# Performance work log

Measured on AMD Instinct MI355X. Metric: run time of the kernel, lower is better.

## Reference

```python
import jax, jax.numpy as jnp
import numpy as np

# Loss hyperparameters (match init_kwargs)
DELTA_VAR = 0.75
DELTA_DIST = 2.0
ALPHA, BETA, GAMMA = 1.0, 1.0, 0.001


def setup_inputs() -> dict:
    key = jax.random.key(0)
    k1, k2 = jax.random.split(key)
    B, C, H, W = 4, 32, 512, 512
    N_INST = 100
    input_ = jax.random.normal(k1, (B, C, H, W), dtype=jnp.float32)
    target = jax.random.randint(k2, (B, 1, H, W), 0, N_INST, dtype=jnp.int64)
    return {"input_": input_, "target": target, "n_instances": N_INST}


def _loss_single(feat, lbl, n_inst):
    # feat: [C, H, W] embeddings for one sample; lbl: [H, W] instance ids in [0, n_inst)
    C = feat.shape[0]
    f = feat.reshape(C, -1).T                     # [P, C] pixel embeddings
    l = lbl.reshape(-1)                           # [P]
    counts = jnp.bincount(l, length=n_inst).astype(f.dtype)     # [n]
    sums = jax.ops.segment_sum(f, l, num_segments=n_inst)       # [n, C]
    means = sums / counts[:, None]                               # cluster means [n, C]

    # variance (attractive) term: hinge on distance of each pixel to its cluster mean
    diff = f - means[l]                           # gather means back to pixels
    var = jnp.linalg.norm(diff, axis=1)           # 'fro' over dim=1 == L2
    var = jnp.clip(var - DELTA_VAR, 0.0) ** 2 / counts[l]
    variance_term = var.sum() / n_inst

    # distance (repulsive) term: hinged pairwise distances between cluster means
    eye = jnp.eye(n_inst, dtype=f.dtype)
    d2 = jnp.sum((means[:, None, :] - means[None, :, :]) ** 2, axis=2)  # [n, n]
    # safe sqrt: diagonal is exactly 0; mask it so grads stay finite, value unchanged
    dmat = jnp.sqrt(jnp.where(d2 > 0, d2, 1.0)) * (1.0 - eye)
    repulsion = 2.0 * DELTA_DIST * (1.0 - eye)
    hinged = jnp.clip(repulsion - dmat, 0.0) ** 2
    distance_term = hinged.sum() / (n_inst * (n_inst - 1))

    # regularization term: pull cluster means toward origin
    reg_term = jnp.linalg.norm(means, axis=1).sum() / n_inst

    return ALPHA * variance_term + BETA * distance_term + GAMMA * reg_term


def reference(input_, target, n_instances):
    # input_: [B, C, H, W], target: [B, 1, H, W]
    lbl = target[:, 0]
    losses = jax.vmap(lambda f, l: _loss_single(f, l, n_instances))(input_, lbl)
    return losses.mean()  # loss.div(n_batches)
```

## Files before the change

kernel.cpp:

```cpp
#include <hip/hip_runtime.h>
#include <math.h>

#define BB 4
#define CC 32
#define HWSZ (512*512)
#define NMAX 128
#define NP 132
#define NP64 133
#define SS (NMAX * CC)

#define PPB 1024
#define CHUNKS (HWSZ / PPB)
#define NBLK (BB * CHUNKS)

#define DSLICE 8

#define DELTA_VAR_C 0.75f
#define DELTA_DIST_C 2.0f
#define GAMMA_C 0.001f
#define FXS 1048576.0f
#define FXI (1.0f / 1048576.0f)
#define BIAS 16777216

#define LD4(p) (*(const float4*)(p))

__device__ __forceinline__ float block_reduce_256(float v, float* red, int tid) {
    #pragma unroll
    for (int o = 32; o > 0; o >>= 1) v += __shfl_down(v, o, 64);
    if ((tid & 63) == 0) red[tid >> 6] = v;
    __syncthreads();
    if (tid == 0) v = red[0] + red[1] + red[2] + red[3];
    return v;
}

__global__ __launch_bounds__(256) void k_seg_sum(
    const float* __restrict__ in, const int* __restrict__ lbl,
    const int* __restrict__ n_ptr, int* __restrict__ sums_i,
    unsigned int* __restrict__ counts_u)
{
    const int N = *n_ptr;
    __shared__ unsigned long long s_sum[(CC / 2) * NP64];
    __shared__ unsigned int s_cnt[NMAX];
    const int tid = threadIdx.x;

    for (int i = tid; i < (CC / 2) * NP64; i += 256) s_sum[i] = 0ull;
    for (int i = tid; i < NMAX; i += 256) s_cnt[i] = 0u;
    __syncthreads();

    const int b = blockIdx.x / CHUNKS;
    const int p0 = (blockIdx.x % CHUNKS) * PPB;

    const int* lb = lbl + (size_t)b * HWSZ + p0 + tid * 4;
    int4 l4 = *(const int4*)(lb);
    int lab[4] = {l4.x, l4.y, l4.z, l4.w};

    #pragma unroll
    for (int i = 0; i < 4; i++) atomicAdd(&s_cnt[lab[i]], 1u);

    const float* p = in + (size_t)b * CC * HWSZ + p0 + (size_t)tid * 4;

    float4 c0a = LD4(p);
    float4 c0b = LD4(p + HWSZ);
    float4 c1a = LD4(p + 2 * (size_t)HWSZ);
    float4 c1b = LD4(p + 3 * (size_t)HWSZ);

    #pragma unroll
    for (int c = 0; c < CC; c += 2) {
        float4 va = c0a, vb = c0b;
        c0a = c1a; c0b = c1b;
        if (c + 4 < CC) {
            const float* q = p + (size_t)(c + 4) * HWSZ;
            c1a = LD4(q);
            c1b = LD4(q + HWSZ);
        }
        float v0[4] = {va.x, va.y, va.z, va.w};
        float v1[4] = {vb.x, vb.y, vb.z, vb.w};
        unsigned long long* row = &s_sum[(c >> 1) * NP64];
        #pragma unroll
        for (int i = 0; i < 4; i++) {
            unsigned int lo = (unsigned int)((int)(v0[i] * FXS) + BIAS);
            unsigned int hi = (unsigned int)((int)(v1[i] * FXS) + BIAS);
            unsigned long long pk = (unsigned long long)lo |
                                    ((unsigned long long)hi << 32);
            atomicAdd(&row[lab[i]], pk);
        }
    }
    __syncthreads();

    for (int i = tid; i < N * CC; i += 256) {
        int n = i / CC, c = i % CC;
        unsigned long long v = s_sum[(c >> 1) * NP64 + n];
        unsigned int half = (c & 1) ? (unsigned int)(v >> 32) : (unsigned int)v;
        long long val = (long long)half - ((long long)s_cnt[n] << 24);
        if (val != 0)
            atomicAdd(&sums_i[(size_t)b * SS + i], (int)val);
    }
    for (int i = tid; i < N; i += 256) {
        unsigned int cv = s_cnt[i];
        if (cv) atomicAdd(&counts_u[b * NMAX + i], cv);
    }
}

__global__ __launch_bounds__(256) void k_var(
    const float* __restrict__ in, const int* __restrict__ lbl,
    const int* __restrict__ n_ptr, const int* __restrict__ sums_i,
    const unsigned int* __restrict__ counts_u, int* __restrict__ out_acc)
{
    const int N = *n_ptr;
    __shared__ float m_t[CC * NP];
    __shared__ float s_invc[NMAX];
    __shared__ float red[4];
    const int tid = threadIdx.x;

    const int b = blockIdx.x / CHUNKS;
    const int chunk = blockIdx.x % CHUNKS;
    const int p0 = chunk * PPB;

    for (int i = tid; i < N; i += 256)
        s_invc[i] = 1.0f / (float)counts_u[b * NMAX + i];
    __syncthreads();
    for (int i = tid; i < N * CC; i += 256) {
        int n = i / CC, c = i % CC;
        m_t[c * NP + n] = (float)sums_i[(size_t)b * SS + i] * FXI * s_invc[n];
    }
    __syncthreads();

    const int* lb = lbl + (size_t)b * HWSZ + p0 + tid * 4;
    int4 l4 = *(const int4*)(lb);
    int lab[4] = {l4.x, l4.y, l4.z, l4.w};
    float acc[4] = {0.f, 0.f, 0.f, 0.f};

    const float* p = in + (size_t)b * CC * HWSZ + p0 + (size_t)tid * 4;
    float4 c0a = LD4(p);
    float4 c0b = LD4(p + HWSZ);
    float4 c1a = LD4(p + 2 * (size_t)HWSZ);
    float4 c1b = LD4(p + 3 * (size_t)HWSZ);

    #pragma unroll
    for (int c = 0; c < CC; c += 2) {
        float4 va = c0a, vb = c0b;
        c0a = c1a; c0b = c1b;
        if (c + 4 < CC) {
            const float* q = p + (size_t)(c + 4) * HWSZ;
            c1a = LD4(q);
            c1b = LD4(q + HWSZ);
        }
        float v0[4] = {va.x, va.y, va.z, va.w};
        #pragma unroll
        for (int i = 0; i < 4; i++) {
            float d = v0[i] - m_t[c * NP + lab[i]];
            acc[i] += d * d;
        }
        float v1[4] = {vb.x, vb.y, vb.z, vb.w};
        #pragma unroll
        for (int i = 0; i < 4; i++) {
            float d = v1[i] - m_t[(c + 1) * NP + lab[i]];
            acc[i] += d * d;
        }
    }

    float vsum = 0.f;
    #pragma unroll
    for (int i = 0; i < 4; i++) {
        float nm = sqrtf(acc[i]);
        float t = fmaxf(nm - DELTA_VAR_C, 0.f);
        vsum += t * t * s_invc[lab[i]];
    }
    float total = vsum * (1.0f / ((float)N * (float)BB));

    if (chunk < DSLICE) {
        float dist_sum = 0.f;
        for (int pr = chunk * 256 + tid; pr < N * N; pr += DSLICE * 256) {
            int i = pr / N, j = pr - i * N;
            if (i == j) continue;
            float d2 = 0.f;
            #pragma unroll
            for (int c = 0; c < CC; c++) {
                float d = m_t[c * NP + i] - m_t[c * NP + j];
                d2 += d * d;
            }
            float dm = (d2 > 0.f) ? sqrtf(d2) : 1.0f;
            float h = fmaxf(2.0f * DELTA_DIST_C - dm, 0.f);
            dist_sum += h * h;
        }
        total += dist_sum * (1.0f / ((float)N * (float)(N - 1) * (float)BB));
        if (chunk == 0) {
            float reg_sum = 0.f;
            for (int n = tid; n < N; n += 256) {
                float s = 0.f;
                #pragma unroll
                for (int c = 0; c < CC; c++) { float v = m_t[c * NP + n]; s += v * v; }
                reg_sum += sqrtf(s);
            }
            total += reg_sum * (GAMMA_C / ((float)N * (float)BB));
        }
    }

    float tot = block_reduce_256(total, red, tid);
    if (tid == 0)
        atomicAdd(out_acc, (int)rintf(tot * FXS));
}

__global__ void k_final(const int* __restrict__ out_acc, float* __restrict__ out) {
    if (threadIdx.x == 0 && blockIdx.x == 0)
        *out = (float)(*out_acc) * FXI;
}

extern "C" void kernel_launch(void* const* d_in, const int* in_sizes, int n_in,
                              void* d_out, int out_size, void* d_ws, size_t ws_size,
                              hipStream_t stream) {
    (void)in_sizes; (void)n_in; (void)out_size; (void)ws_size;
    const float* in  = (const float*)d_in[0];
    const int*   lbl = (const int*)d_in[1];
    const int*   n_ptr = (const int*)d_in[2];
    float* out = (float*)d_out;

    int* sums_i = (int*)d_ws;
    unsigned int* counts_u = (unsigned int*)(sums_i + BB * SS);
    int* out_acc = (int*)(counts_u + BB * NMAX);

    hipMemsetAsync(d_ws, 0, (size_t)(BB * SS + BB * NMAX + 1) * sizeof(int), stream);

    k_seg_sum<<<NBLK, 256, 0, stream>>>(in, lbl, n_ptr, sums_i, counts_u);
    k_var<<<NBLK, 256, 0, stream>>>(in, lbl, n_ptr, sums_i, counts_u, out_acc);
    k_final<<<1, 64, 0, stream>>>(out_acc, out);
}
```

Before: 229.3 us.

## Replace global atomic segment-sum merge with per-block partials and a reduction kernel

Each seg-sum block now writes its full per-cluster partial sums and counts to its own slice of workspace instead of issuing global atomicAdds. A new reduction kernel then sums the 256 chunk partials per batch into the final sums and counts, and also zeroes the output accumulator, which lets the memset be dropped. This is meant to remove contention on global atomics, at the cost of an extra kernel launch and about 17 MB of partial-buffer writes and reads.

```diff
diff --git a/kernel.cpp b/kernel.cpp
--- a/kernel.cpp
+++ b/kernel.cpp
@@ -13,6 +13,9 @@
 #define CHUNKS (HWSZ / PPB)
 #define NBLK (BB * CHUNKS)
 
+#define PSTRIDE (NMAX * CC + NMAX)
+#define RBLK ((PSTRIDE + 255) / 256)
+
 #define DSLICE 8
 
 #define DELTA_VAR_C 0.75f
@@ -35,8 +38,7 @@
 
 __global__ __launch_bounds__(256) void k_seg_sum(
     const float* __restrict__ in, const int* __restrict__ lbl,
-    const int* __restrict__ n_ptr, int* __restrict__ sums_i,
-    unsigned int* __restrict__ counts_u)
+    const int* __restrict__ n_ptr, int* __restrict__ partials)
 {
     const int N = *n_ptr;
     __shared__ unsigned long long s_sum[(CC / 2) * NP64];
@@ -87,18 +89,40 @@
     }
     __syncthreads();
 
+    int* my_part = partials + (size_t)blockIdx.x * PSTRIDE;
     for (int i = tid; i < N * CC; i += 256) {
-        int n = i / CC, c = i % CC;
+        int n = i >> 5, c = i & 31;
         unsigned long long v = s_sum[(c >> 1) * NP64 + n];
         unsigned int half = (c & 1) ? (unsigned int)(v >> 32) : (unsigned int)v;
-        long long val = (long long)half - ((long long)s_cnt[n] << 24);
-        if (val != 0)
-            atomicAdd(&sums_i[(size_t)b * SS + i], (int)val);
-    }
-    for (int i = tid; i < N; i += 256) {
-        unsigned int cv = s_cnt[i];
-        if (cv) atomicAdd(&counts_u[b * NMAX + i], cv);
-    }
+        my_part[i] = (int)((long long)half - ((long long)s_cnt[n] << 24));
+    }
+    for (int i = tid; i < N; i += 256)
+        my_part[NMAX * CC + i] = (int)s_cnt[i];
+}
+
+__global__ __launch_bounds__(256) void k_red(
+    const int* __restrict__ partials, const int* __restrict__ n_ptr,
+    int* __restrict__ sums_i, unsigned int* __restrict__ counts_u,
+    int* __restrict__ out_acc)
+{
+    const int N = *n_ptr;
+    const int tid = threadIdx.x;
+    if (blockIdx.x == 0 && tid == 0) *out_acc = 0;
+
+    const int b = blockIdx.x / RBLK;
+    const int j = (blockIdx.x % RBLK) * 256 + tid;
+    const bool is_sum = (j < N * CC);
+    const bool is_cnt = (j >= NMAX * CC) && (j < NMAX * CC + N);
+    if (!is_sum && !is_cnt) return;
+
+    const int* p = partials + (size_t)b * CHUNKS * PSTRIDE + j;
+    int s = 0;
+    #pragma unroll 8
+    for (int ch = 0; ch < CHUNKS; ch++)
+        s += p[(size_t)ch * PSTRIDE];
+
+    if (is_sum) sums_i[(size_t)b * SS + j] = s;
+    else        counts_u[b * NMAX + (j - NMAX * CC)] = (unsigned int)s;
 }
 
 __global__ __launch_bounds__(256) void k_var(
@@ -120,7 +144,7 @@
         s_invc[i] = 1.0f / (float)counts_u[b * NMAX + i];
     __syncthreads();
     for (int i = tid; i < N * CC; i += 256) {
-        int n = i / CC, c = i % CC;
+        int n = i >> 5, c = i & 31;
         m_t[c * NP + n] = (float)sums_i[(size_t)b * SS + i] * FXI * s_invc[n];
     }
     __syncthreads();
@@ -215,13 +239,13 @@
     const int*   n_ptr = (const int*)d_in[2];
     float* out = (float*)d_out;
 
-    int* sums_i = (int*)d_ws;
+    int* partials = (int*)d_ws;
+    int* sums_i   = partials + (size_t)NBLK * PSTRIDE;
     unsigned int* counts_u = (unsigned int*)(sums_i + BB * SS);
-    int* out_acc = (int*)(counts_u + BB * NMAX);
-
-    hipMemsetAsync(d_ws, 0, (size_t)(BB * SS + BB * NMAX + 1) * sizeof(int), stream);
-
-    k_seg_sum<<<NBLK, 256, 0, stream>>>(in, lbl, n_ptr, sums_i, counts_u);
+    int* out_acc  = (int*)(counts_u + BB * NMAX);
+
+    k_seg_sum<<<NBLK, 256, 0, stream>>>(in, lbl, n_ptr, partials);
+    k_red<<<BB * RBLK, 256, 0, stream>>>(partials, n_ptr, sums_i, counts_u, out_acc);
     k_var<<<NBLK, 256, 0, stream>>>(in, lbl, n_ptr, sums_i, counts_u, out_acc);
     k_final<<<1, 64, 0, stream>>>(out_acc, out);
 }
```

After: 238.0 us. 3.8% more time.

## Fuse segment-sum and variance kernels with per-batch spin barrier and doubled pixels per block

Applied to the files above, without the earlier changes.

Merges the two passes and the final kernel into one persistent-style kernel. Blocks sync per batch through an atomic counter spin-wait, and the last finishing block writes the output. Each block now handles twice as many pixels, and shared memory is unioned between phases to keep two blocks per CU. This removes launch gaps and may let the second read of the chunk hit cache. It relies on all blocks being co-resident, which risks deadlock if occupancy assumptions fail.

```diff
diff --git a/kernel.cpp b/kernel.cpp
--- a/kernel.cpp
+++ b/kernel.cpp
@@ -9,7 +9,7 @@
 #define NP64 133
 #define SS (NMAX * CC)
 
-#define PPB 1024
+#define PPB 2048
 #define CHUNKS (HWSZ / PPB)
 #define NBLK (BB * CHUNKS)
 
@@ -24,6 +24,10 @@
 
 #define LD4(p) (*(const float4*)(p))
 
+struct ShA { unsigned long long s_sum[(CC / 2) * NP64]; unsigned int s_cnt[NMAX]; };
+struct ShC { float m_t[CC * NP]; float s_invc[NMAX]; float red[4]; };
+union ShU { ShA a; ShC c; };
+
 __device__ __forceinline__ float block_reduce_256(float v, float* red, int tid) {
     #pragma unroll
     for (int o = 32; o > 0; o >>= 1) v += __shfl_down(v, o, 64);
@@ -33,51 +37,48 @@
     return v;
 }
 
-__global__ __launch_bounds__(256) void k_seg_sum(
+__global__ __launch_bounds__(256, 2) void k_all(
     const float* __restrict__ in, const int* __restrict__ lbl,
     const int* __restrict__ n_ptr, int* __restrict__ sums_i,
-    unsigned int* __restrict__ counts_u)
+    unsigned int* __restrict__ counts_u, int* __restrict__ done,
+    int* __restrict__ out_acc, float* __restrict__ out)
 {
     const int N = *n_ptr;
-    __shared__ unsigned long long s_sum[(CC / 2) * NP64];
-    __shared__ unsigned int s_cnt[NMAX];
+    __shared__ ShU sh;
     const int tid = threadIdx.x;
-
-    for (int i = tid; i < (CC / 2) * NP64; i += 256) s_sum[i] = 0ull;
-    for (int i = tid; i < NMAX; i += 256) s_cnt[i] = 0u;
-    __syncthreads();
-
     const int b = blockIdx.x / CHUNKS;
-    const int p0 = (blockIdx.x % CHUNKS) * PPB;
-
-    const int* lb = lbl + (size_t)b * HWSZ + p0 + tid * 4;
-    int4 l4 = *(const int4*)(lb);
-    int lab[4] = {l4.x, l4.y, l4.z, l4.w};
+    const int chunk = blockIdx.x % CHUNKS;
+    const int p0 = chunk * PPB;
+
+    for (int i = tid; i < (CC / 2) * NP64; i += 256) sh.a.s_sum[i] = 0ull;
+    for (int i = tid; i < NMAX; i += 256) sh.a.s_cnt[i] = 0u;
+    __syncthreads();
+
+    const int* lb = lbl + (size_t)b * HWSZ + p0 + tid * 8;
+    int4 l4a = *(const int4*)(lb);
+    int4 l4b = *(const int4*)(lb + 4);
+    int lab[8] = {l4a.x, l4a.y, l4a.z, l4a.w, l4b.x, l4b.y, l4b.z, l4b.w};
 
     #pragma unroll
-    for (int i = 0; i < 4; i++) atomicAdd(&s_cnt[lab[i]], 1u);
-
-    const float* p = in + (size_t)b * CC * HWSZ + p0 + (size_t)tid * 4;
-
-    float4 c0a = LD4(p);
-    float4 c0b = LD4(p + HWSZ);
-    float4 c1a = LD4(p + 2 * (size_t)HWSZ);
-    float4 c1b = LD4(p + 3 * (size_t)HWSZ);
-
-    #pragma unroll
+    for (int i = 0; i < 8; i++) atomicAdd(&sh.a.s_cnt[lab[i]], 1u);
+
+    const float* p = in + (size_t)b * CC * HWSZ + p0 + (size_t)tid * 8;
+
+    float4 a0 = LD4(p);            float4 b0 = LD4(p + 4);
+    float4 a1 = LD4(p + HWSZ);     float4 b1 = LD4(p + HWSZ + 4);
+
     for (int c = 0; c < CC; c += 2) {
-        float4 va = c0a, vb = c0b;
-        c0a = c1a; c0b = c1b;
-        if (c + 4 < CC) {
-            const float* q = p + (size_t)(c + 4) * HWSZ;
-            c1a = LD4(q);
-            c1b = LD4(q + HWSZ);
-        }
-        float v0[4] = {va.x, va.y, va.z, va.w};
-        float v1[4] = {vb.x, vb.y, vb.z, vb.w};
-        unsigned long long* row = &s_sum[(c >> 1) * NP64];
+        float4 ca0 = a0, cb0 = b0, ca1 = a1, cb1 = b1;
+        if (c + 2 < CC) {
+            const float* q = p + (size_t)(c + 2) * HWSZ;
+            a0 = LD4(q);          b0 = LD4(q + 4);
+            a1 = LD4(q + HWSZ);   b1 = LD4(q + HWSZ + 4);
+        }
+        float v0[8] = {ca0.x, ca0.y, ca0.z, ca0.w, cb0.x, cb0.y, cb0.z, cb0.w};
+        float v1[8] = {ca1.x, ca1.y, ca1.z, ca1.w, cb1.x, cb1.y, cb1.z, cb1.w};
+        unsigned long long* row = &sh.a.s_sum[(c >> 1) * NP64];
         #pragma unroll
-        for (int i = 0; i < 4; i++) {
+        for (int i = 0; i < 8; i++) {
             unsigned int lo = (unsigned int)((int)(v0[i] * FXS) + BIAS);
             unsigned int hi = (unsigned int)((int)(v1[i] * FXS) + BIAS);
             unsigned long long pk = (unsigned long long)lo |
@@ -88,83 +89,68 @@
     __syncthreads();
 
     for (int i = tid; i < N * CC; i += 256) {
-        int n = i / CC, c = i % CC;
-        unsigned long long v = s_sum[(c >> 1) * NP64 + n];
+        int n = i >> 5, c = i & 31;
+        unsigned long long v = sh.a.s_sum[(c >> 1) * NP64 + n];
         unsigned int half = (c & 1) ? (unsigned int)(v >> 32) : (unsigned int)v;
-        long long val = (long long)half - ((long long)s_cnt[n] << 24);
+        long long val = (long long)half - ((long long)sh.a.s_cnt[n] << 24);
         if (val != 0)
             atomicAdd(&sums_i[(size_t)b * SS + i], (int)val);
     }
     for (int i = tid; i < N; i += 256) {
-        unsigned int cv = s_cnt[i];
+        unsigned int cv = sh.a.s_cnt[i];
         if (cv) atomicAdd(&counts_u[b * NMAX + i], cv);
     }
-}
-
-__global__ __launch_bounds__(256) void k_var(
-    const float* __restrict__ in, const int* __restrict__ lbl,
-    const int* __restrict__ n_ptr, const int* __restrict__ sums_i,
-    const unsigned int* __restrict__ counts_u, int* __restrict__ out_acc)
-{
-    const int N = *n_ptr;
-    __shared__ float m_t[CC * NP];
-    __shared__ float s_invc[NMAX];
-    __shared__ float red[4];
-    const int tid = threadIdx.x;
-
-    const int b = blockIdx.x / CHUNKS;
-    const int chunk = blockIdx.x % CHUNKS;
-    const int p0 = chunk * PPB;
+
+    __threadfence();
+    __syncthreads();
+    if (tid == 0) {
+        atomicAdd(&done[b], 1);
+        while (atomicAdd(&done[b], 0) < CHUNKS) __builtin_amdgcn_s_sleep(16);
+    }
+    __syncthreads();
+    __threadfence();
 
     for (int i = tid; i < N; i += 256)
-        s_invc[i] = 1.0f / (float)counts_u[b * NMAX + i];
+        sh.c.s_invc[i] = 1.0f / (float)counts_u[b * NMAX + i];
     __syncthreads();
     for (int i = tid; i < N * CC; i += 256) {
-        int n = i / CC, c = i % CC;
-        m_t[c * NP + n] = (float)sums_i[(size_t)b * SS + i] * FXI * s_invc[n];
-    }
-    __syncthreads();
-
-    const int* lb = lbl + (size_t)b * HWSZ + p0 + tid * 4;
-    int4 l4 = *(const int4*)(lb);
-    int lab[4] = {l4.x, l4.y, l4.z, l4.w};
-    float acc[4] = {0.f, 0.f, 0.f, 0.f};
-
-    const float* p = in + (size_t)b * CC * HWSZ + p0 + (size_t)tid * 4;
-    float4 c0a = LD4(p);
-    float4 c0b = LD4(p + HWSZ);
-    float4 c1a = LD4(p + 2 * (size_t)HWSZ);
-    float4 c1b = LD4(p + 3 * (size_t)HWSZ);
-
-    #pragma unroll
+        int n = i >> 5, c = i & 31;
+        sh.c.m_t[c * NP + n] = (float)sums_i[(size_t)b * SS + i] * FXI * sh.c.s_invc[n];
+    }
+    __syncthreads();
+
+    float acc[8] = {0.f, 0.f, 0.f, 0.f, 0.f, 0.f, 0.f, 0.f};
+
+    a0 = LD4(p);            b0 = LD4(p + 4);
+    a1 = LD4(p + HWSZ);     b1 = LD4(p + HWSZ + 4);
+
     for (int c = 0; c < CC; c += 2) {
-        float4 va = c0a, vb = c0b;
-        c0a = c1a; c0b = c1b;
-        if (c + 4 < CC) {
-            const float* q = p + (size_t)(c + 4) * HWSZ;
-            c1a = LD4(q);
-            c1b = LD4(q + HWSZ);
-        }
-        float v0[4] = {va.x, va.y, va.z, va.w};
+        float4 ca0 = a0, cb0 = b0, ca1 = a1, cb1 = b1;
+        if (c + 2 < CC) {
+            const float* q = p + (size_t)(c + 2) * HWSZ;
+            a0 = LD4(q);          b0 = LD4(q + 4);
+            a1 = LD4(q + HWSZ);   b1 = LD4(q + HWSZ + 4);
+        }
+        float v0[8] = {ca0.x, ca0.y, ca0.z, ca0.w, cb0.x, cb0.y, cb0.z, cb0.w};
         #pragma unroll
-        for (int i = 0; i < 4; i++) {
-            float d = v0[i] - m_t[c * NP + lab[i]];
+        for (int i = 0; i < 8; i++) {
+            float d = v0[i] - sh.c.m_t[c * NP + lab[i]];
             acc[i] += d * d;
         }
-        float v1[4] = {vb.x, vb.y, vb.z, vb.w};
+        float v1[8] = {ca1.x, ca1.y, ca1.z, ca1.w, cb1.x, cb1.y, cb1.z, cb1.w};
         #pragma unroll
-        for (int i = 0; i < 4; i++) {
-            float d = v1[i] - m_t[(c + 1) * NP + lab[i]];
+        for (int i = 0; i < 8; i++) {
+            float d = v1[i] - sh.c.m_t[(c + 1) * NP + lab[i]];
             acc[i] += d * d;
         }
     }
 
     float vsum = 0.f;
     #pragma unroll
-    for (int i = 0; i < 4; i++) {
+    for (int i = 0; i < 8; i++) {
         float nm = sqrtf(acc[i]);
         float t = fmaxf(nm - DELTA_VAR_C, 0.f);
-        vsum += t * t * s_invc[lab[i]];
+        vsum += t * t * sh.c.s_invc[lab[i]];
     }
     float total = vsum * (1.0f / ((float)N * (float)BB));
 
@@ -176,7 +162,7 @@
             float d2 = 0.f;
             #pragma unroll
             for (int c = 0; c < CC; c++) {
-                float d = m_t[c * NP + i] - m_t[c * NP + j];
+                float d = sh.c.m_t[c * NP + i] - sh.c.m_t[c * NP + j];
                 d2 += d * d;
             }
             float dm = (d2 > 0.f) ? sqrtf(d2) : 1.0f;
@@ -189,21 +175,22 @@
             for (int n = tid; n < N; n += 256) {
                 float s = 0.f;
                 #pragma unroll
-                for (int c = 0; c < CC; c++) { float v = m_t[c * NP + n]; s += v * v; }
+                for (int c = 0; c < CC; c++) { float v = sh.c.m_t[c * NP + n]; s += v * v; }
                 reg_sum += sqrtf(s);
             }
             total += reg_sum * (GAMMA_C / ((float)N * (float)BB));
         }
     }
 
-    float tot = block_reduce_256(total, red, tid);
-    if (tid == 0)
+    float tot = block_reduce_256(total, sh.c.red, tid);
+    if (tid == 0) {
         atomicAdd(out_acc, (int)rintf(tot * FXS));
-}
-
-__global__ void k_final(const int* __restrict__ out_acc, float* __restrict__ out) {
-    if (threadIdx.x == 0 && blockIdx.x == 0)
-        *out = (float)(*out_acc) * FXI;
+        __threadfence();
+        int prev = atomicAdd(&done[BB], 1);
+        if (prev == NBLK - 1) {
+            *out = (float)atomicAdd(out_acc, 0) * FXI;
+        }
+    }
 }
 
 extern "C" void kernel_launch(void* const* d_in, const int* in_sizes, int n_in,
@@ -218,10 +205,11 @@
     int* sums_i = (int*)d_ws;
     unsigned int* counts_u = (unsigned int*)(sums_i + BB * SS);
     int* out_acc = (int*)(counts_u + BB * NMAX);
-
-    hipMemsetAsync(d_ws, 0, (size_t)(BB * SS + BB * NMAX + 1) * sizeof(int), stream);
-
-    k_seg_sum<<<NBLK, 256, 0, stream>>>(in, lbl, n_ptr, sums_i, counts_u);
-    k_var<<<NBLK, 256, 0, stream>>>(in, lbl, n_ptr, sums_i, counts_u, out_acc);
-    k_final<<<1, 64, 0, stream>>>(out_acc, out);
+    int* done    = out_acc + 1;
+
+    hipMemsetAsync(d_ws, 0,
+                   (size_t)(BB * SS + BB * NMAX + 1 + BB + 1) * sizeof(int), stream);
+
+    k_all<<<NBLK, 256, 0, stream>>>(in, lbl, n_ptr, sums_i, counts_u,
+                                    done, out_acc, out);
 }
```

New measurement: 319.2 us. 39.2% more time.
